# Optimization experiments

Hardware: AMD Instinct MI355X
Metric: run time of the kernel (lower is better)

Reference implementation:

```python
import jax, jax.numpy as jnp
import numpy as np

N = 100000   # nodes
E = 1600000  # directed edges (avg degree 16)
D = 128      # num_feature == hidden_channels


def setup_inputs() -> dict:
    key = jax.random.key(0)
    ks = jax.random.split(key, 8)
    s = 1.0 / np.sqrt(D)
    x = jax.random.normal(ks[0], (N, D), jnp.float32)
    edge_index = jax.random.randint(ks[1], (2, E), 0, N, dtype=jnp.int32)
    W1 = jax.random.normal(ks[2], (D, D), jnp.float32) * s
    W2 = jax.random.normal(ks[3], (D, D), jnp.float32) * s
    W3 = jax.random.normal(ks[4], (D, D), jnp.float32) * s
    b1 = jnp.zeros((D,), jnp.float32)
    b2 = jnp.zeros((D,), jnp.float32)
    b3 = jnp.zeros((D,), jnp.float32)
    return {"x": x, "edge_index": edge_index, "W1": W1, "b1": b1,
            "W2": W2, "b2": b2, "W3": W3, "b3": b3}


def reference(x, edge_index, W1, b1, W2, b2, W3, b3):
    # GCNConv with added self-loops and symmetric normalization:
    #   out = D^{-1/2} (A + I) D^{-1/2} (x W) + b
    loops = jnp.arange(N, dtype=edge_index.dtype)
    src = jnp.concatenate([edge_index[0], loops])  # [E+N]
    dst = jnp.concatenate([edge_index[1], loops])
    deg = jax.ops.segment_sum(jnp.ones_like(dst, x.dtype), dst, num_segments=N)
    dinv = jax.lax.rsqrt(deg)                      # deg >= 1 (self-loops)
    norm = dinv[src] * dinv[dst]                   # [E+N]

    def conv(h, W, b):
        h = h @ W                                   # [N, D] dense GEMM
        msg = h[src] * norm[:, None]                # gather + scale [E+N, D]
        return jax.ops.segment_sum(msg, dst, num_segments=N) + b

    # dropout is identity in eval mode
    h = jax.nn.relu(conv(x, W1, b1))
    h = jax.nn.relu(conv(h, W2, b2))
    return conv(h, W3, b3)
```

## Files before the change

kernel.cpp:

```cpp
#include <hip/hip_runtime.h>
#include <hip/hip_fp16.h>

#define DFEAT 128
#define BNODES 256
#define BSHIFT 8
#define B1CHUNK 4096
#define SLABC 8192
#define TPB_TILES 3

typedef _Float16 f16x8 __attribute__((ext_vector_type(8)));
typedef _Float16 f16x4 __attribute__((ext_vector_type(4)));
typedef float f32x4 __attribute__((ext_vector_type(4)));


__global__ __launch_bounds__(256) void bin_k(const int* __restrict__ src, const int* __restrict__ dst,
                                             int* __restrict__ gcnt, unsigned int* __restrict__ slab,
                                             int E, int nbuck) {
    __shared__ int cnt[512];
    __shared__ int off[512];
    __shared__ int gbase[512];
    __shared__ int sd[256];
    __shared__ unsigned int buf[B1CHUNK];
    __shared__ unsigned short bid[B1CHUNK];
    int t = threadIdx.x;
    int base = blockIdx.x * B1CHUNK;
    int nloc = E - base;
    if (nloc > B1CHUNK) nloc = B1CHUNK;
    cnt[t] = 0;
    cnt[t + 256] = 0;
    __syncthreads();
    int k = t;
    for (; k + 768 < nloc; k += 1024) {
        int d0 = dst[base + k], d1 = dst[base + k + 256], d2 = dst[base + k + 512], d3 = dst[base + k + 768];
        atomicAdd(&cnt[d0 >> BSHIFT], 1);
        atomicAdd(&cnt[d1 >> BSHIFT], 1);
        atomicAdd(&cnt[d2 >> BSHIFT], 1);
        atomicAdd(&cnt[d3 >> BSHIFT], 1);
    }
    for (; k < nloc; k += 256) atomicAdd(&cnt[dst[base + k] >> BSHIFT], 1);
    __syncthreads();
    int v0 = cnt[2 * t], v1 = cnt[2 * t + 1];
    int tsum = v0 + v1;
    sd[t] = tsum;
    __syncthreads();
    for (int o = 1; o < 256; o <<= 1) {
        int x = (t >= o) ? sd[t - o] : 0;
        __syncthreads();
        sd[t] += x;
        __syncthreads();
    }
    int texcl = sd[t] - tsum;
    off[2 * t] = texcl;
    off[2 * t + 1] = texcl + v0;
    if (2 * t < nbuck && v0 > 0) gbase[2 * t] = atomicAdd(&gcnt[2 * t], v0);
    if (2 * t + 1 < nbuck && v1 > 0) gbase[2 * t + 1] = atomicAdd(&gcnt[2 * t + 1], v1);
    __syncthreads();
    k = t;
    for (; k + 768 < nloc; k += 1024) {
        int d0 = dst[base + k], d1 = dst[base + k + 256], d2 = dst[base + k + 512], d3 = dst[base + k + 768];
        int s0 = src[base + k], s1 = src[base + k + 256], s2 = src[base + k + 512], s3 = src[base + k + 768];
        int b0 = d0 >> BSHIFT, b1_ = d1 >> BSHIFT, b2_ = d2 >> BSHIFT, b3_ = d3 >> BSHIFT;
        int r0 = atomicAdd(&off[b0], 1); buf[r0] = ((unsigned)s0 << BSHIFT) | (unsigned)(d0 & (BNODES - 1)); bid[r0] = (unsigned short)b0;
        int r1 = atomicAdd(&off[b1_], 1); buf[r1] = ((unsigned)s1 << BSHIFT) | (unsigned)(d1 & (BNODES - 1)); bid[r1] = (unsigned short)b1_;
        int r2 = atomicAdd(&off[b2_], 1); buf[r2] = ((unsigned)s2 << BSHIFT) | (unsigned)(d2 & (BNODES - 1)); bid[r2] = (unsigned short)b2_;
        int r3 = atomicAdd(&off[b3_], 1); buf[r3] = ((unsigned)s3 << BSHIFT) | (unsigned)(d3 & (BNODES - 1)); bid[r3] = (unsigned short)b3_;
    }
    for (; k < nloc; k += 256) {
        int d = dst[base + k];
        int s = src[base + k];
        int b = d >> BSHIFT;
        int r = atomicAdd(&off[b], 1);
        buf[r] = ((unsigned)s << BSHIFT) | (unsigned)(d & (BNODES - 1));
        bid[r] = (unsigned short)b;
    }
    __syncthreads();
    k = t;
    for (; k + 768 < nloc; k += 1024) {
#pragma unroll
        for (int u = 0; u < 4; ++u) {
            int kk = k + u * 256;
            int b = bid[kk];
            int o0 = off[b] - cnt[b];
            int pos = gbase[b] + (kk - o0);
            if (pos < SLABC) slab[(size_t)b * SLABC + pos] = buf[kk];
        }
    }
    for (; k < nloc; k += 256) {
        int b = bid[k];
        int o0 = off[b] - cnt[b];
        int pos = gbase[b] + (k - o0);
        if (pos < SLABC) slab[(size_t)b * SLABC + pos] = buf[k];
    }
}

__global__ __launch_bounds__(256) void bucketAB_k(const unsigned int* __restrict__ slab,
                                                  const int* __restrict__ gcnt,
                                                  int* __restrict__ rp, float* __restrict__ dinv,
                                                  int* __restrict__ cols, int N, int nbuck) {
    __shared__ int cnt[256];
    __shared__ int cur[256];
    __shared__ int psum[256];
    __shared__ int outb[SLABC];
    int t = threadIdx.x;
    int b = blockIdx.x;
    int n0 = b << BSHIFT;
    int nn = N - n0;
    if (nn > BNODES) nn = BNODES;
    int ne_raw = gcnt[b];
    int ne = ne_raw > SLABC ? SLABC : ne_raw;
    const unsigned int* sl = slab + (size_t)b * SLABC;
    int part = 0;
    for (int i = t; i < b; i += 256) part += gcnt[i];
    psum[t] = part;
    cnt[t] = 0;
    __syncthreads();
    for (int o = 128; o > 0; o >>= 1) {
        if (t < o) psum[t] += psum[t + o];
        __syncthreads();
    }
    int base = psum[0];
    int k = t;
    for (; k + 768 < ne; k += 1024) {
        unsigned a0 = sl[k], a1 = sl[k + 256], a2 = sl[k + 512], a3 = sl[k + 768];
        atomicAdd(&cnt[a0 & (BNODES - 1)], 1);
        atomicAdd(&cnt[a1 & (BNODES - 1)], 1);
        atomicAdd(&cnt[a2 & (BNODES - 1)], 1);
        atomicAdd(&cnt[a3 & (BNODES - 1)], 1);
    }
    for (; k < ne; k += 256) atomicAdd(&cnt[sl[k] & (BNODES - 1)], 1);
    __syncthreads();
    int deg = cnt[t];
    for (int o = 1; o < 256; o <<= 1) {
        int x = (t >= o) ? cnt[t - o] : 0;
        __syncthreads();
        cnt[t] += x;
        __syncthreads();
    }
    int excl = cnt[t] - deg;
    if (t < nn) {
        rp[n0 + t] = base + excl;
        dinv[n0 + t] = rsqrtf((float)(deg + 1));
    }
    if (b == nbuck - 1 && t == 0) rp[N] = base + ne_raw;
    cur[t] = excl;
    __syncthreads();
    k = t;
    for (; k + 768 < ne; k += 1024) {
        unsigned a0 = sl[k], a1 = sl[k + 256], a2 = sl[k + 512], a3 = sl[k + 768];
        int p0 = atomicAdd(&cur[a0 & (BNODES - 1)], 1); outb[p0] = (int)(a0 >> BSHIFT);
        int p1 = atomicAdd(&cur[a1 & (BNODES - 1)], 1); outb[p1] = (int)(a1 >> BSHIFT);
        int p2 = atomicAdd(&cur[a2 & (BNODES - 1)], 1); outb[p2] = (int)(a2 >> BSHIFT);
        int p3 = atomicAdd(&cur[a3 & (BNODES - 1)], 1); outb[p3] = (int)(a3 >> BSHIFT);
    }
    for (; k < ne; k += 256) {
        unsigned a = sl[k];
        int p = atomicAdd(&cur[a & (BNODES - 1)], 1);
        outb[p] = (int)(a >> BSHIFT);
    }
    __syncthreads();
    k = t;
    for (; k + 768 < ne; k += 1024) {
        int o0 = outb[k], o1 = outb[k + 256], o2 = outb[k + 512], o3 = outb[k + 768];
        cols[base + k] = o0;
        cols[base + k + 256] = o1;
        cols[base + k + 512] = o2;
        cols[base + k + 768] = o3;
    }
    for (; k < ne; k += 256) cols[base + k] = outb[k];
}

__global__ __launch_bounds__(256) void packW_k(const float* __restrict__ W0, const float* __restrict__ W1,
                                               const float* __restrict__ W2,
                                               const float* __restrict__ b0, const float* __restrict__ b1,
                                               const float* __restrict__ b2,
                                               _Float16* __restrict__ wpk, float* __restrict__ bp) {
    int idx = blockIdx.x * 256 + threadIdx.x;
    int layer = idx >> 14;
    int e = idx & 16383;
    int k = e >> 7;
    int nn = e & 127;
    const float* W = (layer == 0) ? W0 : ((layer == 1) ? W1 : W2);
    int ksrc = (layer == 0) ? k : (((k & 7) << 4) | (k >> 3));
    float v = W[ksrc * DFEAT + nn];
    int kc = k >> 5, quad = (k >> 3) & 3, j = k & 7;
    int ct = nn >> 4;
    int pos = ((ct * 4 + kc) * 64 + quad * 16 + (nn & 15)) * 8 + j;
    wpk[(size_t)layer * 16384 + pos] = (_Float16)v;
    if (idx < 384) {
        int l = idx >> 7, p = idx & 127;
        int c = ((p & 7) << 4) | (p >> 3);
        const float* bb = (l == 0) ? b0 : ((l == 1) ? b1 : b2);
        bp[l * 128 + p] = bb[c];
    }
}


template <typename T> struct LoadV;
template <> struct LoadV<float>  { using T = float4; };
template <> struct LoadV<__half> { using T = f16x4; };

__device__ inline void ldraw(float4& d, const float* p) { d = *(const float4*)p; }
__device__ inline void ldraw(f16x4& d, const __half* p) { d = *(const f16x4*)p; }
__device__ inline void zro(float4& d) { d = make_float4(0.f, 0.f, 0.f, 0.f); }
__device__ inline void zro(f16x4& d) { d = f16x4{(_Float16)0.f, (_Float16)0.f, (_Float16)0.f, (_Float16)0.f}; }
__device__ inline f16x4 cvt4(const float4& v) { return f16x4{(_Float16)v.x, (_Float16)v.y, (_Float16)v.z, (_Float16)v.w}; }
__device__ inline f16x4 cvt4(const f16x4& v) { return v; }

template <typename TIN>
__global__ __launch_bounds__(256) void gemmP_k(const TIN* __restrict__ A, const _Float16* __restrict__ wfrag,
                                               const float* __restrict__ dinv, __half* __restrict__ C,
                                               int n, int ntiles) {
    __shared__ _Float16 al[8192];
    using LV = typename LoadV<TIN>::T;
    const int tid = threadIdx.x;
    const int wv_ = tid >> 6;
    const int lane = tid & 63;
    const int t0 = blockIdx.x * TPB_TILES;
    const int rS = (tid >> 5);
    const int k4 = (tid & 31) * 4;

    LV pre[8];
    {
        int row0 = t0 * 64;
#pragma unroll
        for (int p = 0; p < 8; ++p) {
            int gr = row0 + p * 8 + rS;
            if (gr < n) ldraw(pre[p], &A[(size_t)gr * DFEAT + k4]); else zro(pre[p]);
        }
    }
    for (int tt = 0; tt < TPB_TILES; ++tt) {
        int tile = t0 + tt;
        if (tile >= ntiles) break;
        int row0 = tile * 64;
#pragma unroll
        for (int p = 0; p < 8; ++p) {
            int r = p * 8 + rS;
            int wv2 = r >> 4, m = r & 15;
            int kc = k4 >> 5, quad = (k4 >> 3) & 3, j0 = k4 & 7;
            int dst = ((wv2 * 4 + kc) * 64 + quad * 16 + m) * 8 + j0;
            *(f16x4*)&al[dst] = cvt4(pre[p]);
        }
        __syncthreads();
        if (tt + 1 < TPB_TILES && tile + 1 < ntiles) {
            int nrow0 = (tile + 1) * 64;
#pragma unroll
            for (int p = 0; p < 8; ++p) {
                int gr = nrow0 + p * 8 + rS;
                if (gr < n) ldraw(pre[p], &A[(size_t)gr * DFEAT + k4]); else zro(pre[p]);
            }
        }
        f16x8 af[4];
#pragma unroll
        for (int kc = 0; kc < 4; ++kc)
            af[kc] = *(f16x8*)&al[((wv_ * 4 + kc) * 64 + lane) * 8];
        f32x4 acc[8];
#pragma unroll
        for (int ct = 0; ct < 8; ++ct) acc[ct] = (f32x4){0.f, 0.f, 0.f, 0.f};
#pragma unroll
        for (int ct = 0; ct < 8; ++ct) {
#pragma unroll
            for (int kc = 0; kc < 4; ++kc) {
                f16x8 bf = *(const f16x8*)&wfrag[((size_t)(ct * 4 + kc) * 64 + lane) * 8];
                acc[ct] = __builtin_amdgcn_mfma_f32_16x16x32_f16(af[kc], bf, acc[ct], 0, 0, 0);
            }
        }
        const int quad = lane >> 4, cb = lane & 15;
        const int rbase = row0 + wv_ * 16 + quad * 4;
#pragma unroll
        for (int r = 0; r < 4; ++r) {
            int gr = rbase + r;
            if (gr < n) {
                float dr = dinv[gr];
                f16x8 o;
#pragma unroll
                for (int ct = 0; ct < 8; ++ct) o[ct] = (_Float16)(acc[ct][r] * dr);
                *(f16x8*)&C[(size_t)gr * DFEAT + cb * 8] = o;
            }
        }
        __syncthreads();
    }
}


__device__ inline float2 agg_row(const __half* __restrict__ T, const int* __restrict__ rowptr,
                                 const int* __restrict__ cols, int wid, int lane, int fb) {
    float2 t0 = __half22float2(*(const __half2*)(T + (size_t)wid * DFEAT + fb));
    float ax = t0.x;
    float ay = t0.y;
    int s = rowptr[wid], e = rowptr[wid + 1];
    for (int p = s; p < e; ) {
        int take = e - p;
        if (take > 64) take = 64;
        int q = p + lane;
        if (q >= e) q = e - 1;
        int ci = cols[q];
        int j = 0;
        for (; j + 8 <= take; j += 8) {
            int c0 = __builtin_amdgcn_readlane(ci, j + 0);
            int c1 = __builtin_amdgcn_readlane(ci, j + 1);
            int c2 = __builtin_amdgcn_readlane(ci, j + 2);
            int c3 = __builtin_amdgcn_readlane(ci, j + 3);
            int c4 = __builtin_amdgcn_readlane(ci, j + 4);
            int c5 = __builtin_amdgcn_readlane(ci, j + 5);
            int c6 = __builtin_amdgcn_readlane(ci, j + 6);
            int c7 = __builtin_amdgcn_readlane(ci, j + 7);
            float2 v0 = __half22float2(*(const __half2*)(T + (size_t)c0 * DFEAT + fb));
            float2 v1 = __half22float2(*(const __half2*)(T + (size_t)c1 * DFEAT + fb));
            float2 v2 = __half22float2(*(const __half2*)(T + (size_t)c2 * DFEAT + fb));
            float2 v3 = __half22float2(*(const __half2*)(T + (size_t)c3 * DFEAT + fb));
            float2 v4 = __half22float2(*(const __half2*)(T + (size_t)c4 * DFEAT + fb));
            float2 v5 = __half22float2(*(const __half2*)(T + (size_t)c5 * DFEAT + fb));
            float2 v6 = __half22float2(*(const __half2*)(T + (size_t)c6 * DFEAT + fb));
            float2 v7 = __half22float2(*(const __half2*)(T + (size_t)c7 * DFEAT + fb));
            ax += v0.x; ay += v0.y;
            ax += v1.x; ay += v1.y;
            ax += v2.x; ay += v2.y;
            ax += v3.x; ay += v3.y;
            ax += v4.x; ay += v4.y;
            ax += v5.x; ay += v5.y;
            ax += v6.x; ay += v6.y;
            ax += v7.x; ay += v7.y;
        }
        for (; j < take; ++j) {
            int c = __builtin_amdgcn_readlane(ci, j);
            float2 v = __half22float2(*(const __half2*)(T + (size_t)c * DFEAT + fb));
            ax += v.x; ay += v.y;
        }
        p += take;
    }
    return make_float2(ax, ay);
}

__global__ __launch_bounds__(256) void agg_k(const __half* __restrict__ T, const float* __restrict__ dinv,
                                             const int* __restrict__ rowptr, const int* __restrict__ cols,
                                             const float* __restrict__ biasp,
                                             __half* __restrict__ out, int n) {
    int wid = (int)((blockIdx.x * (size_t)blockDim.x + threadIdx.x) >> 6);
    int lane = threadIdx.x & 63;
    if (wid >= n) return;
    int fb = lane * 2;
    float2 a = agg_row(T, rowptr, cols, wid, lane, fb);
    float dw = dinv[wid];
    float ox = fmaxf(dw * a.x + biasp[fb], 0.f);
    float oy = fmaxf(dw * a.y + biasp[fb + 1], 0.f);
    *(__half2*)(out + (size_t)wid * DFEAT + fb) = __floats2half2_rn(ox, oy);
}

__global__ __launch_bounds__(256) void aggF_k(const __half* __restrict__ T, const float* __restrict__ dinv,
                                              const int* __restrict__ rowptr, const int* __restrict__ cols,
                                              const float* __restrict__ biasp,
                                              float* __restrict__ out, int n) {
    int wid = (int)((blockIdx.x * (size_t)blockDim.x + threadIdx.x) >> 6);
    int lane = threadIdx.x & 63;
    if (wid >= n) return;
    int fb = lane * 2;
    float2 a = agg_row(T, rowptr, cols, wid, lane, fb);
    float dw = dinv[wid];
    float ox = dw * a.x + biasp[fb];
    float oy = dw * a.y + biasp[fb + 1];
    int c0 = ((fb & 7) << 4) | (fb >> 3);
    int c1 = (((fb + 1) & 7) << 4) | ((fb + 1) >> 3);
    out[(size_t)wid * DFEAT + c0] = ox;
    out[(size_t)wid * DFEAT + c1] = oy;
}


extern "C" void kernel_launch(void* const* d_in, const int* in_sizes, int n_in,
                              void* d_out, int out_size, void* d_ws, size_t ws_size,
                              hipStream_t stream) {
    const float* x  = (const float*)d_in[0];
    const int*   ei = (const int*)d_in[1];
    const float* W1 = (const float*)d_in[2];
    const float* b1 = (const float*)d_in[3];
    const float* W2 = (const float*)d_in[4];
    const float* b2 = (const float*)d_in[5];
    const float* W3 = (const float*)d_in[6];
    const float* b3 = (const float*)d_in[7];
    float* out = (float*)d_out;

    const int N = in_sizes[0] / DFEAT;
    const int E = in_sizes[1] / 2;
    const int* srcp = ei;
    const int* dstp = ei + E;

    size_t off = 0;
    auto alloc = [&](size_t bytes) -> void* {
        void* p = (char*)d_ws + off;
        off += (bytes + 255) & ~(size_t)255;
        return p;
    };
    const int nbuck = (N + BNODES - 1) / BNODES;

    int*    gcnt = (int*)alloc(2048);
    int*    rp   = (int*)alloc((size_t)(N + 1) * 4);
    float*  dinv = (float*)alloc((size_t)N * 4);
    _Float16* wpk = (_Float16*)alloc((size_t)3 * 16384 * 2);
    float*  bp   = (float*)alloc(3 * 128 * 4);
    unsigned int* slab = (unsigned int*)alloc((size_t)nbuck * SLABC * 4);
    int*    cols = (int*)alloc((size_t)E * 4);
    __half* bufA = (__half*)alloc((size_t)N * DFEAT * 2);
    __half* bufB = (__half*)alloc((size_t)N * DFEAT * 2);

    packW_k<<<192, 256, 0, stream>>>(W1, W2, W3, b1, b2, b3, wpk, bp);
    hipMemsetAsync(gcnt, 0, 2048, stream);
    bin_k<<<(E + B1CHUNK - 1) / B1CHUNK, 256, 0, stream>>>(srcp, dstp, gcnt, slab, E, nbuck);
    bucketAB_k<<<nbuck, 256, 0, stream>>>(slab, gcnt, rp, dinv, cols, N, nbuck);

    int ntiles = (N + 63) / 64;
    int gemmGrid = (ntiles + TPB_TILES - 1) / TPB_TILES;
    int aggGrid  = (int)(((size_t)N * 64 + 255) / 256);

    gemmP_k<float><<<gemmGrid, 256, 0, stream>>>(x, wpk, dinv, bufA, N, ntiles);
    agg_k<<<aggGrid, 256, 0, stream>>>(bufA, dinv, rp, cols, bp, bufB, N);

    gemmP_k<__half><<<gemmGrid, 256, 0, stream>>>(bufB, wpk + 16384, dinv, bufA, N, ntiles);
    agg_k<<<aggGrid, 256, 0, stream>>>(bufA, dinv, rp, cols, bp + 128, bufB, N);

    gemmP_k<__half><<<gemmGrid, 256, 0, stream>>>(bufB, wpk + 32768, dinv, bufA, N, ntiles);
    aggF_k<<<aggGrid, 256, 0, stream>>>(bufA, dinv, rp, cols, bp + 256, out, N);
}
```

Measured before the change: 403.7 us.

## Stage GEMM weights in LDS, swizzle A tile layout, fold memset into packW

The GEMM kernel now copies the packed 128x128 fp16 weight fragments into shared memory once per block, so MFMA operands are read from LDS instead of global memory. A rows are loaded as 8-wide fp16 chunks with an XOR swizzle to avoid LDS bank conflicts, and dinv is prefetched before the MFMA loop. Tiles per block drop from 3 to 2. The gcnt memset is folded into packW_k to remove one API call. The cost is 32 KB of extra LDS per block, which may reduce occupancy, plus the weight copy repeated in every block.

```diff
diff --git a/kernel.cpp b/kernel.cpp
--- a/kernel.cpp
+++ b/kernel.cpp
@@ -6,7 +6,7 @@
 #define BSHIFT 8
 #define B1CHUNK 4096
 #define SLABC 8192
-#define TPB_TILES 3
+#define TPB_TILES 2
 
 typedef _Float16 f16x8 __attribute__((ext_vector_type(8)));
 typedef _Float16 f16x4 __attribute__((ext_vector_type(4)));
@@ -173,7 +173,8 @@
                                                const float* __restrict__ W2,
                                                const float* __restrict__ b0, const float* __restrict__ b1,
                                                const float* __restrict__ b2,
-                                               _Float16* __restrict__ wpk, float* __restrict__ bp) {
+                                               _Float16* __restrict__ wpk, float* __restrict__ bp,
+                                               int* __restrict__ gcnt) {
     int idx = blockIdx.x * 256 + threadIdx.x;
     int layer = idx >> 14;
     int e = idx & 16383;
@@ -192,40 +193,47 @@
         const float* bb = (l == 0) ? b0 : ((l == 1) ? b1 : b2);
         bp[l * 128 + p] = bb[c];
     }
-}
-
-
-template <typename T> struct LoadV;
-template <> struct LoadV<float>  { using T = float4; };
-template <> struct LoadV<__half> { using T = f16x4; };
-
-__device__ inline void ldraw(float4& d, const float* p) { d = *(const float4*)p; }
-__device__ inline void ldraw(f16x4& d, const __half* p) { d = *(const f16x4*)p; }
-__device__ inline void zro(float4& d) { d = make_float4(0.f, 0.f, 0.f, 0.f); }
-__device__ inline void zro(f16x4& d) { d = f16x4{(_Float16)0.f, (_Float16)0.f, (_Float16)0.f, (_Float16)0.f}; }
-__device__ inline f16x4 cvt4(const float4& v) { return f16x4{(_Float16)v.x, (_Float16)v.y, (_Float16)v.z, (_Float16)v.w}; }
-__device__ inline f16x4 cvt4(const f16x4& v) { return v; }
+    if (idx < 512) gcnt[idx] = 0;
+}
+
+
+__device__ inline f16x8 ldA8(const float* p) {
+    float4 a = *(const float4*)p;
+    float4 b = *(const float4*)(p + 4);
+    return f16x8{(_Float16)a.x, (_Float16)a.y, (_Float16)a.z, (_Float16)a.w,
+                 (_Float16)b.x, (_Float16)b.y, (_Float16)b.z, (_Float16)b.w};
+}
+__device__ inline f16x8 ldA8(const __half* p) { return *(const f16x8*)p; }
+__device__ inline f16x8 zero8() {
+    return f16x8{(_Float16)0.f, (_Float16)0.f, (_Float16)0.f, (_Float16)0.f,
+                 (_Float16)0.f, (_Float16)0.f, (_Float16)0.f, (_Float16)0.f};
+}
 
 template <typename TIN>
 __global__ __launch_bounds__(256) void gemmP_k(const TIN* __restrict__ A, const _Float16* __restrict__ wfrag,
                                                const float* __restrict__ dinv, __half* __restrict__ C,
                                                int n, int ntiles) {
     __shared__ _Float16 al[8192];
-    using LV = typename LoadV<TIN>::T;
+    __shared__ _Float16 wl[16384];
     const int tid = threadIdx.x;
     const int wv_ = tid >> 6;
     const int lane = tid & 63;
     const int t0 = blockIdx.x * TPB_TILES;
-    const int rS = (tid >> 5);
-    const int k4 = (tid & 31) * 4;
-
-    LV pre[8];
+    const int chunk = tid & 15;
+    const int rsub = tid >> 4;
+    const int kcS = chunk >> 2, quadS = chunk & 3;
+    const int swzS = (kcS << 1) ^ (quadS & 1);
+
+    for (int c = tid; c < 2048; c += 256)
+        *(f16x8*)&wl[c * 8] = *(const f16x8*)&wfrag[c * 8];
+
+    f16x8 pre[4];
     {
         int row0 = t0 * 64;
 #pragma unroll
-        for (int p = 0; p < 8; ++p) {
-            int gr = row0 + p * 8 + rS;
-            if (gr < n) ldraw(pre[p], &A[(size_t)gr * DFEAT + k4]); else zro(pre[p]);
+        for (int p = 0; p < 4; ++p) {
+            int gr = row0 + p * 16 + rsub;
+            pre[p] = (gr < n) ? ldA8(&A[(size_t)gr * DFEAT + chunk * 8]) : zero8();
         }
     }
     for (int tt = 0; tt < TPB_TILES; ++tt) {
@@ -233,26 +241,31 @@
         if (tile >= ntiles) break;
         int row0 = tile * 64;
 #pragma unroll
-        for (int p = 0; p < 8; ++p) {
-            int r = p * 8 + rS;
-            int wv2 = r >> 4, m = r & 15;
-            int kc = k4 >> 5, quad = (k4 >> 3) & 3, j0 = k4 & 7;
-            int dst = ((wv2 * 4 + kc) * 64 + quad * 16 + m) * 8 + j0;
-            *(f16x4*)&al[dst] = cvt4(pre[p]);
+        for (int p = 0; p < 4; ++p) {
+            int idx = (p * 4 + kcS) * 64 + quadS * 16 + rsub;
+            *(f16x8*)&al[(idx ^ swzS) * 8] = pre[p];
         }
         __syncthreads();
         if (tt + 1 < TPB_TILES && tile + 1 < ntiles) {
             int nrow0 = (tile + 1) * 64;
 #pragma unroll
-            for (int p = 0; p < 8; ++p) {
-                int gr = nrow0 + p * 8 + rS;
-                if (gr < n) ldraw(pre[p], &A[(size_t)gr * DFEAT + k4]); else zro(pre[p]);
+            for (int p = 0; p < 4; ++p) {
+                int gr = nrow0 + p * 16 + rsub;
+                pre[p] = (gr < n) ? ldA8(&A[(size_t)gr * DFEAT + chunk * 8]) : zero8();
             }
         }
         f16x8 af[4];
-#pragma unroll
-        for (int kc = 0; kc < 4; ++kc)
-            af[kc] = *(f16x8*)&al[((wv_ * 4 + kc) * 64 + lane) * 8];
+        const int swzR = (lane >> 4) & 1;
+#pragma unroll
+        for (int kc = 0; kc < 4; ++kc) {
+            int idx = (wv_ * 4 + kc) * 64 + lane;
+            af[kc] = *(f16x8*)&al[(idx ^ (kc << 1) ^ swzR) * 8];
+        }
+        const int quad = lane >> 4, cb = lane & 15;
+        const int rbase = row0 + wv_ * 16 + quad * 4;
+        float ds[4];
+#pragma unroll
+        for (int r = 0; r < 4; ++r) ds[r] = (rbase + r < n) ? dinv[rbase + r] : 0.f;
         f32x4 acc[8];
 #pragma unroll
         for (int ct = 0; ct < 8; ++ct) acc[ct] = (f32x4){0.f, 0.f, 0.f, 0.f};
@@ -260,20 +273,17 @@
         for (int ct = 0; ct < 8; ++ct) {
 #pragma unroll
             for (int kc = 0; kc < 4; ++kc) {
-                f16x8 bf = *(const f16x8*)&wfrag[((size_t)(ct * 4 + kc) * 64 + lane) * 8];
+                f16x8 bf = *(f16x8*)&wl[((ct * 4 + kc) * 64 + lane) * 8];
                 acc[ct] = __builtin_amdgcn_mfma_f32_16x16x32_f16(af[kc], bf, acc[ct], 0, 0, 0);
             }
         }
-        const int quad = lane >> 4, cb = lane & 15;
-        const int rbase = row0 + wv_ * 16 + quad * 4;
 #pragma unroll
         for (int r = 0; r < 4; ++r) {
             int gr = rbase + r;
             if (gr < n) {
-                float dr = dinv[gr];
                 f16x8 o;
 #pragma unroll
-                for (int ct = 0; ct < 8; ++ct) o[ct] = (_Float16)(acc[ct][r] * dr);
+                for (int ct = 0; ct < 8; ++ct) o[ct] = (_Float16)(acc[ct][r] * ds[r]);
                 *(f16x8*)&C[(size_t)gr * DFEAT + cb * 8] = o;
             }
         }
@@ -401,8 +411,7 @@
     __half* bufA = (__half*)alloc((size_t)N * DFEAT * 2);
     __half* bufB = (__half*)alloc((size_t)N * DFEAT * 2);
 
-    packW_k<<<192, 256, 0, stream>>>(W1, W2, W3, b1, b2, b3, wpk, bp);
-    hipMemsetAsync(gcnt, 0, 2048, stream);
+    packW_k<<<192, 256, 0, stream>>>(W1, W2, W3, b1, b2, b3, wpk, bp, gcnt);
     bin_k<<<(E + B1CHUNK - 1) / B1CHUNK, 256, 0, stream>>>(srcp, dstp, gcnt, slab, E, nbuck);
     bucketAB_k<<<nbuck, 256, 0, stream>>>(slab, gcnt, rp, dinv, cols, N, nbuck);
 
```

New measurement: 379.4 us. -6.0%, faster.
